# Kernel tuning notes

Measured on AMD Instinct MI355X. Metric: run time of the kernel, lower is better.

The kernel has to match this reference:

```python
import jax, jax.numpy as jnp
import numpy as np

NEG_SLOPE = 0.1  # leaky_relu slope used by Conv1dNormRelu in the repo


def grid_sample_bilinear(feat, xy):
    """Bilinear sample feat [B,C,H,W] at pixel coords xy [B,2,N].

    Equivalent to the repo's grid_sample_wrapper: it normalizes xy to [-1,1]
    and calls F.grid_sample(align_corners=True, padding_mode='zeros'), which
    maps back to exactly these pixel coordinates. Out-of-bounds corners -> 0.
    Returns [B,C,N].
    """
    B, C, H, W = feat.shape
    x = xy[:, 0]  # [B,N]
    y = xy[:, 1]
    x0 = jnp.floor(x)
    y0 = jnp.floor(y)
    wx1 = x - x0
    wy1 = y - y0
    wx0 = 1.0 - wx1
    wy0 = 1.0 - wy1

    def gather(ix, iy):
        valid = (ix >= 0) & (ix <= W - 1) & (iy >= 0) & (iy <= H - 1)
        ixc = jnp.clip(ix, 0, W - 1).astype(jnp.int32)
        iyc = jnp.clip(iy, 0, H - 1).astype(jnp.int32)
        # per-batch gather: f[:, iy, ix] -> [C, N]
        v = jax.vmap(lambda f, iy_, ix_: f[:, iy_, ix_])(feat, iyc, ixc)  # [B,C,N]
        return v * valid[:, None, :].astype(feat.dtype)

    out = (gather(x0, y0) * (wx0 * wy0)[:, None, :]
           + gather(x0 + 1, y0) * (wx1 * wy0)[:, None, :]
           + gather(x0, y0 + 1) * (wx0 * wy1)[:, None, :]
           + gather(x0 + 1, y0 + 1) * (wx1 * wy1)[:, None, :])
    return out


def setup_inputs() -> dict:
    key = jax.random.key(0)
    k1, k2, k3, k4 = jax.random.split(key, 4)
    B, N = 4, 16384
    C2D, C3D, H, W_img = 128, 128, 96, 160
    # pixel coords in [0, W-1] x [0, H-1]
    u = jax.random.uniform(k1, (B, 1, N), dtype=jnp.float32) * (W_img - 1)
    v = jax.random.uniform(k2, (B, 1, N), dtype=jnp.float32) * (H - 1)
    xy = jnp.concatenate([u, v], axis=1)  # [B,2,N]
    feat_2d = jax.random.normal(k3, (B, C2D, H, W_img), dtype=jnp.float32)
    feat_3d = jax.random.normal(k4, (B, C3D, N), dtype=jnp.float32)
    kw, kb = jax.random.split(jax.random.fold_in(key, 7))
    fan_in = C2D + C3D
    W = jax.random.normal(kw, (C3D, fan_in), dtype=jnp.float32) / np.sqrt(fan_in)
    b = jnp.zeros((C3D,), dtype=jnp.float32)
    return {"xy": xy, "feat_2d": feat_2d, "feat_3d": feat_3d, "W": W, "b": b}


def reference(xy, feat_2d, feat_3d, W, b):
    # torch.no_grad() around the gather -> stop_gradient
    feat_2d_to_3d = jax.lax.stop_gradient(grid_sample_bilinear(feat_2d, xy))  # [B,C2d,N]
    cat = jnp.concatenate([feat_2d_to_3d, feat_3d], axis=1)  # [B,C2d+C3d,N]
    # Conv1d with kernel_size=1 == pointwise matmul over channels
    y = jnp.einsum('oi,bin->bon', W, cat) + b[None, :, None]
    return jnp.where(y >= 0, y, NEG_SLOPE * y)
```

## Files before the change

kernel.cpp:

```cpp
#include <hip/hip_runtime.h>
#include <hip/hip_bf16.h>

#define NSAMP 16384
#define BB    4
#define C2D   128
#define C3D   128
#define HH    96
#define WW    160
#define COUT  128
#define KK    256
#define TN    64
#define HW    (HH*WW)
#define CATS  264

typedef __attribute__((ext_vector_type(8))) short bf16x8;
typedef __attribute__((ext_vector_type(4))) float f32x4;

__device__ __forceinline__ float bf16lo(unsigned int u) { return __uint_as_float(u << 16); }
__device__ __forceinline__ float bf16hi(unsigned int u) { return __uint_as_float(u & 0xffff0000u); }
__device__ __forceinline__ unsigned int pack2(float a, float b) {
    union { __hip_bfloat162 h; unsigned int u; } c;
    c.h = __float22bfloat162_rn(make_float2(a, b));
    return c.u;
}

__global__ __launch_bounds__(256) void transpose_cvt_kernel(
    const float* __restrict__ f2d, unsigned short* __restrict__ f2dt)
{
    __shared__ unsigned short t[64 * 66];
    const int tid  = threadIdx.x;
    const int lane = tid & 63;
    const int wv   = tid >> 6;
    const int blk  = blockIdx.x;
    const int b    = blk / ((HW / 64) * 2);
    const int rem  = blk % ((HW / 64) * 2);
    const int c0   = (rem & 1) * 64;
    const int hw0  = (rem >> 1) * 64;

    #pragma unroll
    for (int s = 0; s < 16; ++s) {
        const int cl = s * 4 + wv;
        float v = f2d[(size_t)(b * C2D + c0 + cl) * HW + hw0 + lane];
        __hip_bfloat16 h = __float2bfloat16(v);
        t[lane * 66 + cl] = *(unsigned short*)&h;
    }
    __syncthreads();
    const unsigned int* tw  = (const unsigned int*)t;
    unsigned int*       wsu = (unsigned int*)f2dt;
    #pragma unroll
    for (int s = 0; s < 8; ++s) {
        const int hwl = s * 8 + (tid >> 5);
        const int cu  = tid & 31;
        wsu[((size_t)(b * HW + hw0 + hwl) * C2D + c0) / 2 + cu] = tw[hwl * 33 + cu];
    }
}

__global__ __launch_bounds__(256) void wcvt_kernel(
    const float* __restrict__ Wm, unsigned short* __restrict__ Wb)
{
    const int i = blockIdx.x * 256 + threadIdx.x;
    const float4 v = ((const float4*)Wm)[i];
    uint2 o;
    o.x = pack2(v.x, v.y);
    o.y = pack2(v.z, v.w);
    ((uint2*)Wb)[i] = o;
}

__global__ __launch_bounds__(256, 4) void fuse_kernel(
    const float*          __restrict__ xy,
    const unsigned short* __restrict__ f2dt,
    const float*          __restrict__ f3d,
    const unsigned short* __restrict__ Wb,
    const float*          __restrict__ bias,
    float* __restrict__ out)
{
    __shared__ unsigned short cat[TN * CATS];
    __shared__ float4 sw4[TN];
    __shared__ int4   soff4[TN];

    const int tid  = threadIdx.x;
    const int lane = tid & 63;
    const int wv   = tid >> 6;
    const int blk  = blockIdx.x;
    const int b    = blk >> 8;
    const int n0   = (blk & 255) * TN;

    if (tid < TN) {
        const int n = n0 + tid;
        float x = xy[((size_t)b * 2 + 0) * NSAMP + n];
        float y = xy[((size_t)b * 2 + 1) * NSAMP + n];
        float xf = floorf(x), yf = floorf(y);
        float wx1 = x - xf, wy1 = y - yf;
        float wx0 = 1.0f - wx1, wy0 = 1.0f - wy1;
        int x0 = (int)xf, y0 = (int)yf;
        int x1 = x0 + 1, y1 = y0 + 1;
        if (x0 < 0 || x0 > WW - 1) wx0 = 0.0f;
        if (x1 < 0 || x1 > WW - 1) wx1 = 0.0f;
        if (y0 < 0 || y0 > HH - 1) wy0 = 0.0f;
        if (y1 < 0 || y1 > HH - 1) wy1 = 0.0f;
        x0 = min(max(x0, 0), WW - 1);
        x1 = min(max(x1, 0), WW - 1);
        y0 = min(max(y0, 0), HH - 1);
        y1 = min(max(y1, 0), HH - 1);
        sw4[tid]   = make_float4(wx0 * wy0, wx1 * wy0, wx0 * wy1, wx1 * wy1);
        soff4[tid] = make_int4(y0 * WW + x0, y0 * WW + x1,
                               y1 * WW + x0, y1 * WW + x1);
    }
    __syncthreads();

    unsigned int* catw = (unsigned int*)cat;

    {
        const float* p3 = f3d + (size_t)(b * C3D) * NSAMP + n0 + lane;
        #pragma unroll
        for (int ch = 0; ch < 4; ++ch) {
            const int cbase = wv * 32 + ch * 8;
            float v[8];
            #pragma unroll
            for (int t = 0; t < 8; ++t) v[t] = p3[(size_t)(cbase + t) * NSAMP];
            uint4 pk;
            pk.x = pack2(v[0], v[1]);
            pk.y = pack2(v[2], v[3]);
            pk.z = pack2(v[4], v[5]);
            pk.w = pack2(v[6], v[7]);
            *(uint4*)&catw[lane * (CATS / 2) + (C2D / 2) + (cbase >> 1)] = pk;
        }
    }

    {
        const int s   = lane >> 5;
        const int ch4 = (lane & 31) * 4;
        const unsigned short* fb = f2dt + (size_t)b * HW * C2D + ch4;
        #pragma unroll 4
        for (int i = 0; i < 8; ++i) {
            const int j = wv * 16 + i * 2 + s;
            const float4 w = sw4[j];
            const int4   o = soff4[j];
            const uint2 c0v = *(const uint2*)(fb + (size_t)o.x * C2D);
            const uint2 c1v = *(const uint2*)(fb + (size_t)o.y * C2D);
            const uint2 c2v = *(const uint2*)(fb + (size_t)o.z * C2D);
            const uint2 c3v = *(const uint2*)(fb + (size_t)o.w * C2D);
            float r0 = w.x * bf16lo(c0v.x) + w.y * bf16lo(c1v.x)
                     + w.z * bf16lo(c2v.x) + w.w * bf16lo(c3v.x);
            float r1 = w.x * bf16hi(c0v.x) + w.y * bf16hi(c1v.x)
                     + w.z * bf16hi(c2v.x) + w.w * bf16hi(c3v.x);
            float r2 = w.x * bf16lo(c0v.y) + w.y * bf16lo(c1v.y)
                     + w.z * bf16lo(c2v.y) + w.w * bf16lo(c3v.y);
            float r3 = w.x * bf16hi(c0v.y) + w.y * bf16hi(c1v.y)
                     + w.z * bf16hi(c2v.y) + w.w * bf16hi(c3v.y);
            uint2 pk;
            pk.x = pack2(r0, r1);
            pk.y = pack2(r2, r3);
            *(uint2*)&catw[j * (CATS / 2) + (ch4 >> 1)] = pk;
        }
    }
    __syncthreads();

    {
        const int quad = lane >> 4;
        const int nloc = lane & 15;

        f32x4 acc[2][4];
        #pragma unroll
        for (int mt = 0; mt < 2; ++mt)
            #pragma unroll
            for (int nt = 0; nt < 4; ++nt)
                acc[mt][nt] = (f32x4){0.f, 0.f, 0.f, 0.f};

        const unsigned short* wb0 = Wb + (size_t)(wv * 32 + nloc) * KK + quad * 8;

        #pragma unroll 2
        for (int ks = 0; ks < 8; ++ks) {
            const int k0 = ks * 32;
            const bf16x8 a0 = *(const bf16x8*)(wb0 + k0);
            const bf16x8 a1 = *(const bf16x8*)(wb0 + 16 * KK + k0);
            #pragma unroll
            for (int nt = 0; nt < 4; ++nt) {
                const bf16x8 bfrag = *(const bf16x8*)
                    &cat[(nt * 16 + nloc) * CATS + k0 + quad * 8];
                acc[0][nt] = __builtin_amdgcn_mfma_f32_16x16x32_bf16(
                    a0, bfrag, acc[0][nt], 0, 0, 0);
                acc[1][nt] = __builtin_amdgcn_mfma_f32_16x16x32_bf16(
                    a1, bfrag, acc[1][nt], 0, 0, 0);
            }
        }

        #pragma unroll
        for (int mt = 0; mt < 2; ++mt) {
            const int cobase = wv * 32 + mt * 16 + quad * 4;
            float bv[4];
            #pragma unroll
            for (int r = 0; r < 4; ++r) bv[r] = bias[cobase + r];
            #pragma unroll
            for (int nt = 0; nt < 4; ++nt) {
                float* po = out + (size_t)(b * COUT + cobase) * NSAMP
                          + n0 + nt * 16 + nloc;
                #pragma unroll
                for (int r = 0; r < 4; ++r) {
                    float yv = acc[mt][nt][r] + bv[r];
                    yv = (yv >= 0.0f) ? yv : 0.1f * yv;
                    po[(size_t)r * NSAMP] = yv;
                }
            }
        }
    }
}

extern "C" void kernel_launch(void* const* d_in, const int* in_sizes, int n_in,
                              void* d_out, int out_size, void* d_ws, size_t ws_size,
                              hipStream_t stream) {
    const float* xy   = (const float*)d_in[0];
    const float* f2d  = (const float*)d_in[1];
    const float* f3d  = (const float*)d_in[2];
    const float* Wm   = (const float*)d_in[3];
    const float* bias = (const float*)d_in[4];
    float* out = (float*)d_out;

    unsigned short* f2dt = (unsigned short*)d_ws;
    unsigned short* Wb   = f2dt + (size_t)BB * HW * C2D;

    wcvt_kernel<<<dim3((COUT * KK / 4) / 256), 256, 0, stream>>>(Wm, Wb);
    transpose_cvt_kernel<<<dim3(BB * (HW / 64) * 2), 256, 0, stream>>>(f2d, f2dt);
    fuse_kernel<<<dim3(BB * (NSAMP / TN)), 256, 0, stream>>>(
        xy, f2dt, f3d, Wb, bias, out);
}
```

Baseline: 128.6 us.

## Project 2D features before bilinear sampling and fuse interpolation into accumulators

Uses linearity of bilinear sampling to apply the 2D half of the pointwise weights to the image feature map first, producing a projected bf16 map. The fuse kernel then runs an MFMA only over the 3D features and adds bilinearly interpolated projected values directly into the accumulators, removing the shared-memory staging of sampled 2D features. The separate transpose kernel is replaced by the projection kernel, and the tile size drops to 32 samples with a block-order swizzle. Rounding the projected values to bf16 slightly changes the numerics.

Result: slower. 166.8 us (+29.7%).

```diff
diff --git a/kernel.cpp b/kernel.cpp
--- a/kernel.cpp
+++ b/kernel.cpp
@@ -8,10 +8,9 @@
 #define HH    96
 #define WW    160
 #define COUT  128
-#define KK    256
-#define TN    64
 #define HW    (HH*WW)
-#define CATS  264
+#define TN    32
+#define PROW  136
 
 typedef __attribute__((ext_vector_type(8))) short bf16x8;
 typedef __attribute__((ext_vector_type(4))) float f32x4;
@@ -24,66 +23,100 @@
     return c.u;
 }
 
-__global__ __launch_bounds__(256) void transpose_cvt_kernel(
-    const float* __restrict__ f2d, unsigned short* __restrict__ f2dt)
-{
-    __shared__ unsigned short t[64 * 66];
-    const int tid  = threadIdx.x;
-    const int lane = tid & 63;
-    const int wv   = tid >> 6;
-    const int blk  = blockIdx.x;
-    const int b    = blk / ((HW / 64) * 2);
-    const int rem  = blk % ((HW / 64) * 2);
-    const int c0   = (rem & 1) * 64;
-    const int hw0  = (rem >> 1) * 64;
-
-    #pragma unroll
-    for (int s = 0; s < 16; ++s) {
-        const int cl = s * 4 + wv;
-        float v = f2d[(size_t)(b * C2D + c0 + cl) * HW + hw0 + lane];
-        __hip_bfloat16 h = __float2bfloat16(v);
-        t[lane * 66 + cl] = *(unsigned short*)&h;
-    }
-    __syncthreads();
-    const unsigned int* tw  = (const unsigned int*)t;
-    unsigned int*       wsu = (unsigned int*)f2dt;
-    #pragma unroll
-    for (int s = 0; s < 8; ++s) {
-        const int hwl = s * 8 + (tid >> 5);
-        const int cu  = tid & 31;
-        wsu[((size_t)(b * HW + hw0 + hwl) * C2D + c0) / 2 + cu] = tw[hwl * 33 + cu];
-    }
-}
-
 __global__ __launch_bounds__(256) void wcvt_kernel(
-    const float* __restrict__ Wm, unsigned short* __restrict__ Wb)
+    const float* __restrict__ Wm,
+    unsigned short* __restrict__ Wb2, unsigned short* __restrict__ Wb3)
 {
     const int i = blockIdx.x * 256 + threadIdx.x;
     const float4 v = ((const float4*)Wm)[i];
     uint2 o;
     o.x = pack2(v.x, v.y);
     o.y = pack2(v.z, v.w);
-    ((uint2*)Wb)[i] = o;
-}
-
-__global__ __launch_bounds__(256, 4) void fuse_kernel(
-    const float*          __restrict__ xy,
-    const unsigned short* __restrict__ f2dt,
-    const float*          __restrict__ f3d,
-    const unsigned short* __restrict__ Wb,
-    const float*          __restrict__ bias,
-    float* __restrict__ out)
+    const int co = i >> 6;
+    const int c4 = i & 63;
+    unsigned short* dst = (c4 < 32) ? (Wb2 + co * 128 + c4 * 4)
+                                    : (Wb3 + co * 128 + (c4 - 32) * 4);
+    *(uint2*)dst = o;
+}
+
+__global__ __launch_bounds__(256, 4) void proj2d_kernel(
+    const float*          __restrict__ f2d,
+    const unsigned short* __restrict__ Wb2,
+    unsigned short*       __restrict__ P)
 {
-    __shared__ unsigned short cat[TN * CATS];
-    __shared__ float4 sw4[TN];
-    __shared__ int4   soff4[TN];
-
+    __shared__ unsigned short t[64 * PROW];
     const int tid  = threadIdx.x;
     const int lane = tid & 63;
     const int wv   = tid >> 6;
     const int blk  = blockIdx.x;
-    const int b    = blk >> 8;
-    const int n0   = (blk & 255) * TN;
+    const int b    = blk / (HW / 64);
+    const int hw0  = (blk % (HW / 64)) * 64;
+
+    const float* src = f2d + (size_t)b * C2D * HW + hw0 + lane;
+    #pragma unroll
+    for (int g = 0; g < 4; ++g) {
+        const int c0 = wv * 32 + g * 8;
+        float v[8];
+        #pragma unroll
+        for (int k = 0; k < 8; ++k) v[k] = src[(size_t)(c0 + k) * HW];
+        uint4 pk;
+        pk.x = pack2(v[0], v[1]);
+        pk.y = pack2(v[2], v[3]);
+        pk.z = pack2(v[4], v[5]);
+        pk.w = pack2(v[6], v[7]);
+        *(uint4*)&t[lane * PROW + c0] = pk;
+    }
+    __syncthreads();
+
+    const int quad = lane >> 4;
+    const int nloc = lane & 15;
+
+    f32x4 acc[8];
+    #pragma unroll
+    for (int nt = 0; nt < 8; ++nt) acc[nt] = (f32x4){0.f, 0.f, 0.f, 0.f};
+
+    const unsigned short* arow = &t[(wv * 16 + nloc) * PROW + quad * 8];
+    const unsigned short* brow = Wb2 + nloc * 128 + quad * 8;
+
+    #pragma unroll
+    for (int ks = 0; ks < 4; ++ks) {
+        const bf16x8 a = *(const bf16x8*)(arow + ks * 32);
+        #pragma unroll
+        for (int nt = 0; nt < 8; ++nt) {
+            const bf16x8 bb = *(const bf16x8*)(brow + nt * 16 * 128 + ks * 32);
+            acc[nt] = __builtin_amdgcn_mfma_f32_16x16x32_bf16(a, bb, acc[nt], 0, 0, 0);
+        }
+    }
+
+    unsigned short* pb = P + ((size_t)b * HW + hw0 + wv * 16 + quad * 4) * C2D + nloc;
+    #pragma unroll
+    for (int nt = 0; nt < 8; ++nt) {
+        #pragma unroll
+        for (int r = 0; r < 4; ++r) {
+            __hip_bfloat16 h = __float2bfloat16(acc[nt][r]);
+            pb[(size_t)r * C2D + nt * 16] = *(unsigned short*)&h;
+        }
+    }
+}
+
+__global__ __launch_bounds__(256, 6) void fuse_kernel(
+    const float*          __restrict__ xy,
+    const unsigned short* __restrict__ P,
+    const float*          __restrict__ f3d,
+    const unsigned short* __restrict__ Wb3,
+    const float*          __restrict__ bias,
+    float* __restrict__ out)
+{
+    __shared__ unsigned short cat3[TN * PROW];
+    __shared__ float4 sw4[TN];
+    __shared__ int4   soff4[TN];
+
+    const int tid  = threadIdx.x;
+    const int lane = tid & 63;
+    const int wv   = tid >> 6;
+    const int blk  = (blockIdx.x & 7) * 256 + (blockIdx.x >> 3);
+    const int b    = blk >> 9;
+    const int n0   = (blk & 511) * TN;
 
     if (tid < TN) {
         const int n = n0 + tid;
@@ -106,101 +139,95 @@
         soff4[tid] = make_int4(y0 * WW + x0, y0 * WW + x1,
                                y1 * WW + x0, y1 * WW + x1);
     }
+
+    {
+        const int s  = tid & 31;
+        const int cg = tid >> 5;
+        const float* p3 = f3d + ((size_t)(b * C3D + cg * 16)) * NSAMP + n0 + s;
+        float v[16];
+        #pragma unroll
+        for (int k = 0; k < 16; ++k) v[k] = p3[(size_t)k * NSAMP];
+        uint4 pk0, pk1;
+        pk0.x = pack2(v[0],  v[1]);  pk0.y = pack2(v[2],  v[3]);
+        pk0.z = pack2(v[4],  v[5]);  pk0.w = pack2(v[6],  v[7]);
+        pk1.x = pack2(v[8],  v[9]);  pk1.y = pack2(v[10], v[11]);
+        pk1.z = pack2(v[12], v[13]); pk1.w = pack2(v[14], v[15]);
+        *(uint4*)&cat3[s * PROW + cg * 16]     = pk0;
+        *(uint4*)&cat3[s * PROW + cg * 16 + 8] = pk1;
+    }
     __syncthreads();
 
-    unsigned int* catw = (unsigned int*)cat;
+    const int quad = lane >> 4;
+    const int nloc = lane & 15;
+
+    f32x4 acc[2][2];
+    #pragma unroll
+    for (int mt = 0; mt < 2; ++mt)
+        #pragma unroll
+        for (int nt = 0; nt < 2; ++nt)
+            acc[mt][nt] = (f32x4){0.f, 0.f, 0.f, 0.f};
 
     {
-        const float* p3 = f3d + (size_t)(b * C3D) * NSAMP + n0 + lane;
-        #pragma unroll
-        for (int ch = 0; ch < 4; ++ch) {
-            const int cbase = wv * 32 + ch * 8;
-            float v[8];
-            #pragma unroll
-            for (int t = 0; t < 8; ++t) v[t] = p3[(size_t)(cbase + t) * NSAMP];
-            uint4 pk;
-            pk.x = pack2(v[0], v[1]);
-            pk.y = pack2(v[2], v[3]);
-            pk.z = pack2(v[4], v[5]);
-            pk.w = pack2(v[6], v[7]);
-            *(uint4*)&catw[lane * (CATS / 2) + (C2D / 2) + (cbase >> 1)] = pk;
-        }
-    }
-
-    {
-        const int s   = lane >> 5;
-        const int ch4 = (lane & 31) * 4;
-        const unsigned short* fb = f2dt + (size_t)b * HW * C2D + ch4;
-        #pragma unroll 4
-        for (int i = 0; i < 8; ++i) {
-            const int j = wv * 16 + i * 2 + s;
-            const float4 w = sw4[j];
-            const int4   o = soff4[j];
-            const uint2 c0v = *(const uint2*)(fb + (size_t)o.x * C2D);
-            const uint2 c1v = *(const uint2*)(fb + (size_t)o.y * C2D);
-            const uint2 c2v = *(const uint2*)(fb + (size_t)o.z * C2D);
-            const uint2 c3v = *(const uint2*)(fb + (size_t)o.w * C2D);
-            float r0 = w.x * bf16lo(c0v.x) + w.y * bf16lo(c1v.x)
-                     + w.z * bf16lo(c2v.x) + w.w * bf16lo(c3v.x);
-            float r1 = w.x * bf16hi(c0v.x) + w.y * bf16hi(c1v.x)
-                     + w.z * bf16hi(c2v.x) + w.w * bf16hi(c3v.x);
-            float r2 = w.x * bf16lo(c0v.y) + w.y * bf16lo(c1v.y)
-                     + w.z * bf16lo(c2v.y) + w.w * bf16lo(c3v.y);
-            float r3 = w.x * bf16hi(c0v.y) + w.y * bf16hi(c1v.y)
-                     + w.z * bf16hi(c2v.y) + w.w * bf16hi(c3v.y);
-            uint2 pk;
-            pk.x = pack2(r0, r1);
-            pk.y = pack2(r2, r3);
-            *(uint2*)&catw[j * (CATS / 2) + (ch4 >> 1)] = pk;
-        }
-    }
-    __syncthreads();
-
-    {
-        const int quad = lane >> 4;
-        const int nloc = lane & 15;
-
-        f32x4 acc[2][4];
-        #pragma unroll
-        for (int mt = 0; mt < 2; ++mt)
-            #pragma unroll
-            for (int nt = 0; nt < 4; ++nt)
-                acc[mt][nt] = (f32x4){0.f, 0.f, 0.f, 0.f};
-
-        const unsigned short* wb0 = Wb + (size_t)(wv * 32 + nloc) * KK + quad * 8;
-
-        #pragma unroll 2
-        for (int ks = 0; ks < 8; ++ks) {
+        const unsigned short* wb0 = Wb3 + (wv * 32 + nloc) * 128 + quad * 8;
+        #pragma unroll
+        for (int ks = 0; ks < 4; ++ks) {
             const int k0 = ks * 32;
             const bf16x8 a0 = *(const bf16x8*)(wb0 + k0);
-            const bf16x8 a1 = *(const bf16x8*)(wb0 + 16 * KK + k0);
+            const bf16x8 a1 = *(const bf16x8*)(wb0 + 16 * 128 + k0);
             #pragma unroll
-            for (int nt = 0; nt < 4; ++nt) {
+            for (int nt = 0; nt < 2; ++nt) {
                 const bf16x8 bfrag = *(const bf16x8*)
-                    &cat[(nt * 16 + nloc) * CATS + k0 + quad * 8];
+                    &cat3[(nt * 16 + nloc) * PROW + k0 + quad * 8];
                 acc[0][nt] = __builtin_amdgcn_mfma_f32_16x16x32_bf16(
                     a0, bfrag, acc[0][nt], 0, 0, 0);
                 acc[1][nt] = __builtin_amdgcn_mfma_f32_16x16x32_bf16(
                     a1, bfrag, acc[1][nt], 0, 0, 0);
             }
         }
-
-        #pragma unroll
-        for (int mt = 0; mt < 2; ++mt) {
-            const int cobase = wv * 32 + mt * 16 + quad * 4;
-            float bv[4];
+    }
+
+    {
+        const unsigned short* pb = P + (size_t)b * HW * C2D;
+        #pragma unroll
+        for (int nt = 0; nt < 2; ++nt) {
+            const int j = nt * 16 + nloc;
+            const float4 w = sw4[j];
+            const int4   o = soff4[j];
             #pragma unroll
-            for (int r = 0; r < 4; ++r) bv[r] = bias[cobase + r];
+            for (int mt = 0; mt < 2; ++mt) {
+                const int cobase = wv * 32 + mt * 16 + quad * 4;
+                const unsigned short* pc = pb + cobase;
+                const uint2 c0v = *(const uint2*)(pc + (size_t)o.x * C2D);
+                const uint2 c1v = *(const uint2*)(pc + (size_t)o.y * C2D);
+                const uint2 c2v = *(const uint2*)(pc + (size_t)o.z * C2D);
+                const uint2 c3v = *(const uint2*)(pc + (size_t)o.w * C2D);
+                acc[mt][nt][0] += w.x * bf16lo(c0v.x) + w.y * bf16lo(c1v.x)
+                                + w.z * bf16lo(c2v.x) + w.w * bf16lo(c3v.x);
+                acc[mt][nt][1] += w.x * bf16hi(c0v.x) + w.y * bf16hi(c1v.x)
+                                + w.z * bf16hi(c2v.x) + w.w * bf16hi(c3v.x);
+                acc[mt][nt][2] += w.x * bf16lo(c0v.y) + w.y * bf16lo(c1v.y)
+                                + w.z * bf16lo(c2v.y) + w.w * bf16lo(c3v.y);
+                acc[mt][nt][3] += w.x * bf16hi(c0v.y) + w.y * bf16hi(c1v.y)
+                                + w.z * bf16hi(c2v.y) + w.w * bf16hi(c3v.y);
+            }
+        }
+    }
+
+    #pragma unroll
+    for (int mt = 0; mt < 2; ++mt) {
+        const int cobase = wv * 32 + mt * 16 + quad * 4;
+        float bv[4];
+        #pragma unroll
+        for (int r = 0; r < 4; ++r) bv[r] = bias[cobase + r];
+        #pragma unroll
+        for (int nt = 0; nt < 2; ++nt) {
+            float* po = out + (size_t)(b * COUT + cobase) * NSAMP
+                      + n0 + nt * 16 + nloc;
             #pragma unroll
-            for (int nt = 0; nt < 4; ++nt) {
-                float* po = out + (size_t)(b * COUT + cobase) * NSAMP
-                          + n0 + nt * 16 + nloc;
-                #pragma unroll
-                for (int r = 0; r < 4; ++r) {
-                    float yv = acc[mt][nt][r] + bv[r];
-                    yv = (yv >= 0.0f) ? yv : 0.1f * yv;
-                    po[(size_t)r * NSAMP] = yv;
-                }
+            for (int r = 0; r < 4; ++r) {
+                float yv = acc[mt][nt][r] + bv[r];
+                yv = (yv >= 0.0f) ? yv : 0.1f * yv;
+                po[(size_t)r * NSAMP] = yv;
             }
         }
     }
@@ -216,11 +243,12 @@
     const float* bias = (const float*)d_in[4];
     float* out = (float*)d_out;
 
-    unsigned short* f2dt = (unsigned short*)d_ws;
-    unsigned short* Wb   = f2dt + (size_t)BB * HW * C2D;
-
-    wcvt_kernel<<<dim3((COUT * KK / 4) / 256), 256, 0, stream>>>(Wm, Wb);
-    transpose_cvt_kernel<<<dim3(BB * (HW / 64) * 2), 256, 0, stream>>>(f2d, f2dt);
+    unsigned short* P   = (unsigned short*)d_ws;
+    unsigned short* Wb2 = P + (size_t)BB * HW * C2D;
+    unsigned short* Wb3 = Wb2 + (size_t)COUT * 128;
+
+    wcvt_kernel<<<dim3((COUT * 256 / 4) / 256), 256, 0, stream>>>(Wm, Wb2, Wb3);
+    proj2d_kernel<<<dim3(BB * (HW / 64)), 256, 0, stream>>>(f2d, Wb2, P);
     fuse_kernel<<<dim3(BB * (NSAMP / TN)), 256, 0, stream>>>(
-        xy, f2dt, f3d, Wb, bias, out);
-}
+        xy, P, f3d, Wb3, bias, out);
+}
```

## Overlap gather with MFMA on feat_3d half and widen kernels to 512 threads

Applied to the files above, without the earlier changes.

The fused kernel now runs 512 threads per block. Bilinear weights and offsets stay in registers and are broadcast with shuffles instead of going through shared memory. The MFMA over the feat_3d half of K runs while the 2D gather loads are in flight, and the 2D half is blended and multiplied after a second barrier. The transpose kernel is rewritten to handle 128 pixels by all channels per block with XOR-swizzled shared memory and 16-byte stores. Both kernels also remap block indices, presumably to spread consecutive blocks across XCDs. The cost is higher register pressure from the prefetched gathers and an extra barrier.

Result: slower. 135.5 us (+5.3%).

```diff
diff --git a/kernel.cpp b/kernel.cpp
--- a/kernel.cpp
+++ b/kernel.cpp
@@ -9,9 +9,10 @@
 #define WW    160
 #define COUT  128
 #define KK    256
+#define HW    (HH*WW)
 #define TN    64
-#define HW    (HH*WW)
 #define CATS  264
+#define TS    136
 
 typedef __attribute__((ext_vector_type(8))) short bf16x8;
 typedef __attribute__((ext_vector_type(4))) float f32x4;
@@ -24,37 +25,6 @@
     return c.u;
 }
 
-__global__ __launch_bounds__(256) void transpose_cvt_kernel(
-    const float* __restrict__ f2d, unsigned short* __restrict__ f2dt)
-{
-    __shared__ unsigned short t[64 * 66];
-    const int tid  = threadIdx.x;
-    const int lane = tid & 63;
-    const int wv   = tid >> 6;
-    const int blk  = blockIdx.x;
-    const int b    = blk / ((HW / 64) * 2);
-    const int rem  = blk % ((HW / 64) * 2);
-    const int c0   = (rem & 1) * 64;
-    const int hw0  = (rem >> 1) * 64;
-
-    #pragma unroll
-    for (int s = 0; s < 16; ++s) {
-        const int cl = s * 4 + wv;
-        float v = f2d[(size_t)(b * C2D + c0 + cl) * HW + hw0 + lane];
-        __hip_bfloat16 h = __float2bfloat16(v);
-        t[lane * 66 + cl] = *(unsigned short*)&h;
-    }
-    __syncthreads();
-    const unsigned int* tw  = (const unsigned int*)t;
-    unsigned int*       wsu = (unsigned int*)f2dt;
-    #pragma unroll
-    for (int s = 0; s < 8; ++s) {
-        const int hwl = s * 8 + (tid >> 5);
-        const int cu  = tid & 31;
-        wsu[((size_t)(b * HW + hw0 + hwl) * C2D + c0) / 2 + cu] = tw[hwl * 33 + cu];
-    }
-}
-
 __global__ __launch_bounds__(256) void wcvt_kernel(
     const float* __restrict__ Wm, unsigned short* __restrict__ Wb)
 {
@@ -66,7 +36,59 @@
     ((uint2*)Wb)[i] = o;
 }
 
-__global__ __launch_bounds__(256, 4) void fuse_kernel(
+__global__ __launch_bounds__(512) void transpose_cvt_kernel(
+    const float* __restrict__ f2d, unsigned short* __restrict__ f2dt)
+{
+    __shared__ unsigned short t[128 * TS];
+    unsigned int* tw = (unsigned int*)t;
+    const int tid  = threadIdx.x;
+    const int lane = tid & 63;
+    const int wv   = tid >> 6;
+    const int blk  = (blockIdx.x & 7) * 60 + (blockIdx.x >> 3);
+    const int b    = blk / 120;
+    const int hw0  = (blk % 120) * 128;
+
+    const int xk = 4 * ((lane >> 3) & 7);
+    const float* src = f2d + (size_t)b * C2D * HW + hw0 + lane;
+    #pragma unroll
+    for (int st = 0; st < 8; ++st) {
+        const int c = wv * 16 + st * 2;
+        const float va0 = src[(size_t)c * HW];
+        const float vb0 = src[(size_t)(c + 1) * HW];
+        const float va1 = src[(size_t)c * HW + 64];
+        const float vb1 = src[(size_t)(c + 1) * HW + 64];
+        const int w = (c >> 1) ^ xk;
+        tw[lane        * (TS / 2) + w] = pack2(va0, vb0);
+        tw[(lane + 64) * (TS / 2) + w] = pack2(va1, vb1);
+    }
+    __syncthreads();
+    #pragma unroll
+    for (int it = 0; it < 4; ++it) {
+        const int r  = it * 32 + (tid >> 4);
+        const int rk = 4 * ((r >> 3) & 7);
+        const uint4 v = *(const uint4*)&tw[r * (TS / 2) + (((tid & 15) * 4) ^ rk)];
+        *(uint4*)&f2dt[((size_t)b * HW + hw0 + r) * C2D + (tid & 15) * 8] = v;
+    }
+}
+
+__device__ __forceinline__ void blend_write(
+    const uint2* cv, const float4 bw, unsigned int* catw, int row, int ch4)
+{
+    float r0 = bw.x * bf16lo(cv[0].x) + bw.y * bf16lo(cv[1].x)
+             + bw.z * bf16lo(cv[2].x) + bw.w * bf16lo(cv[3].x);
+    float r1 = bw.x * bf16hi(cv[0].x) + bw.y * bf16hi(cv[1].x)
+             + bw.z * bf16hi(cv[2].x) + bw.w * bf16hi(cv[3].x);
+    float r2 = bw.x * bf16lo(cv[0].y) + bw.y * bf16lo(cv[1].y)
+             + bw.z * bf16lo(cv[2].y) + bw.w * bf16lo(cv[3].y);
+    float r3 = bw.x * bf16hi(cv[0].y) + bw.y * bf16hi(cv[1].y)
+             + bw.z * bf16hi(cv[2].y) + bw.w * bf16hi(cv[3].y);
+    uint2 pk;
+    pk.x = pack2(r0, r1);
+    pk.y = pack2(r2, r3);
+    *(uint2*)&catw[row * (CATS / 2) + (ch4 >> 1)] = pk;
+}
+
+__global__ __launch_bounds__(512, 4) void fuse_kernel(
     const float*          __restrict__ xy,
     const unsigned short* __restrict__ f2dt,
     const float*          __restrict__ f3d,
@@ -75,18 +97,19 @@
     float* __restrict__ out)
 {
     __shared__ unsigned short cat[TN * CATS];
-    __shared__ float4 sw4[TN];
-    __shared__ int4   soff4[TN];
+    unsigned int* catw = (unsigned int*)cat;
 
     const int tid  = threadIdx.x;
     const int lane = tid & 63;
     const int wv   = tid >> 6;
-    const int blk  = blockIdx.x;
+    const int blk  = (blockIdx.x & 7) * 128 + (blockIdx.x >> 3);
     const int b    = blk >> 8;
     const int n0   = (blk & 255) * TN;
 
-    if (tid < TN) {
-        const int n = n0 + tid;
+    float w4x, w4y, w4z, w4w;
+    int   o4x, o4y, o4z, o4w;
+    {
+        const int n = n0 + wv * 8 + (lane & 7);
         float x = xy[((size_t)b * 2 + 0) * NSAMP + n];
         float y = xy[((size_t)b * 2 + 1) * NSAMP + n];
         float xf = floorf(x), yf = floorf(y);
@@ -102,105 +125,127 @@
         x1 = min(max(x1, 0), WW - 1);
         y0 = min(max(y0, 0), HH - 1);
         y1 = min(max(y1, 0), HH - 1);
-        sw4[tid]   = make_float4(wx0 * wy0, wx1 * wy0, wx0 * wy1, wx1 * wy1);
-        soff4[tid] = make_int4(y0 * WW + x0, y0 * WW + x1,
-                               y1 * WW + x0, y1 * WW + x1);
+        w4x = wx0 * wy0; w4y = wx1 * wy0; w4z = wx0 * wy1; w4w = wx1 * wy1;
+        o4x = y0 * WW + x0; o4y = y0 * WW + x1;
+        o4z = y1 * WW + x0; o4w = y1 * WW + x1;
+    }
+
+    float v3[16];
+    {
+        const float* p3 = f3d + ((size_t)(b * C3D + wv * 16)) * NSAMP + n0 + lane;
+        #pragma unroll
+        for (int t = 0; t < 16; ++t) v3[t] = p3[(size_t)t * NSAMP];
+    }
+
+    const int s2  = lane >> 5;
+    const int ch4 = (lane & 31) * 4;
+    const unsigned short* fb = f2dt + (size_t)b * HW * C2D + ch4;
+    uint2  ga[2][4];
+    float4 wA[2];
+    #pragma unroll
+    for (int i = 0; i < 2; ++i) {
+        const int src = i * 2 + s2;
+        int4 o;
+        o.x = __shfl(o4x, src); o.y = __shfl(o4y, src);
+        o.z = __shfl(o4z, src); o.w = __shfl(o4w, src);
+        wA[i].x = __shfl(w4x, src); wA[i].y = __shfl(w4y, src);
+        wA[i].z = __shfl(w4z, src); wA[i].w = __shfl(w4w, src);
+        ga[i][0] = *(const uint2*)(fb + (size_t)o.x * C2D);
+        ga[i][1] = *(const uint2*)(fb + (size_t)o.y * C2D);
+        ga[i][2] = *(const uint2*)(fb + (size_t)o.z * C2D);
+        ga[i][3] = *(const uint2*)(fb + (size_t)o.w * C2D);
+    }
+
+    {
+        uint4 pk0, pk1;
+        pk0.x = pack2(v3[0],  v3[1]);  pk0.y = pack2(v3[2],  v3[3]);
+        pk0.z = pack2(v3[4],  v3[5]);  pk0.w = pack2(v3[6],  v3[7]);
+        pk1.x = pack2(v3[8],  v3[9]);  pk1.y = pack2(v3[10], v3[11]);
+        pk1.z = pack2(v3[12], v3[13]); pk1.w = pack2(v3[14], v3[15]);
+        *(uint4*)&catw[lane * (CATS / 2) + (C2D / 2) + wv * 8]     = pk0;
+        *(uint4*)&catw[lane * (CATS / 2) + (C2D / 2) + wv * 8 + 4] = pk1;
     }
     __syncthreads();
 
-    unsigned int* catw = (unsigned int*)cat;
-
-    {
-        const float* p3 = f3d + (size_t)(b * C3D) * NSAMP + n0 + lane;
-        #pragma unroll
-        for (int ch = 0; ch < 4; ++ch) {
-            const int cbase = wv * 32 + ch * 8;
-            float v[8];
+    const int quad = lane >> 4;
+    const int nloc = lane & 15;
+    const int mwv  = (wv & 3) * 32;
+    const int nwv  = (wv >> 2) * 32;
+
+    f32x4 acc[2][2];
+    #pragma unroll
+    for (int mt = 0; mt < 2; ++mt)
+        #pragma unroll
+        for (int nt = 0; nt < 2; ++nt)
+            acc[mt][nt] = (f32x4){0.f, 0.f, 0.f, 0.f};
+
+    const unsigned short* wb0 = Wb + (size_t)(mwv + nloc) * KK + quad * 8;
+
+    #pragma unroll
+    for (int ks = 4; ks < 8; ++ks) {
+        const int k0 = ks * 32;
+        const bf16x8 a0 = *(const bf16x8*)(wb0 + k0);
+        const bf16x8 a1 = *(const bf16x8*)(wb0 + 16 * KK + k0);
+        #pragma unroll
+        for (int nt = 0; nt < 2; ++nt) {
+            const bf16x8 bf = *(const bf16x8*)
+                &cat[(nwv + nt * 16 + nloc) * CATS + k0 + quad * 8];
+            acc[0][nt] = __builtin_amdgcn_mfma_f32_16x16x32_bf16(a0, bf, acc[0][nt], 0, 0, 0);
+            acc[1][nt] = __builtin_amdgcn_mfma_f32_16x16x32_bf16(a1, bf, acc[1][nt], 0, 0, 0);
+        }
+    }
+
+    uint2  gb[2][4];
+    float4 wB[2];
+    #pragma unroll
+    for (int i = 0; i < 2; ++i) {
+        const int src = (i + 2) * 2 + s2;
+        int4 o;
+        o.x = __shfl(o4x, src); o.y = __shfl(o4y, src);
+        o.z = __shfl(o4z, src); o.w = __shfl(o4w, src);
+        wB[i].x = __shfl(w4x, src); wB[i].y = __shfl(w4y, src);
+        wB[i].z = __shfl(w4z, src); wB[i].w = __shfl(w4w, src);
+        gb[i][0] = *(const uint2*)(fb + (size_t)o.x * C2D);
+        gb[i][1] = *(const uint2*)(fb + (size_t)o.y * C2D);
+        gb[i][2] = *(const uint2*)(fb + (size_t)o.z * C2D);
+        gb[i][3] = *(const uint2*)(fb + (size_t)o.w * C2D);
+        blend_write(ga[i], wA[i], catw, wv * 8 + i * 2 + s2, ch4);
+    }
+    #pragma unroll
+    for (int i = 0; i < 2; ++i) {
+        blend_write(gb[i], wB[i], catw, wv * 8 + (i + 2) * 2 + s2, ch4);
+    }
+    __syncthreads();
+
+    #pragma unroll
+    for (int ks = 0; ks < 4; ++ks) {
+        const int k0 = ks * 32;
+        const bf16x8 a0 = *(const bf16x8*)(wb0 + k0);
+        const bf16x8 a1 = *(const bf16x8*)(wb0 + 16 * KK + k0);
+        #pragma unroll
+        for (int nt = 0; nt < 2; ++nt) {
+            const bf16x8 bf = *(const bf16x8*)
+                &cat[(nwv + nt * 16 + nloc) * CATS + k0 + quad * 8];
+            acc[0][nt] = __builtin_amdgcn_mfma_f32_16x16x32_bf16(a0, bf, acc[0][nt], 0, 0, 0);
+            acc[1][nt] = __builtin_amdgcn_mfma_f32_16x16x32_bf16(a1, bf, acc[1][nt], 0, 0, 0);
+        }
+    }
+
+    #pragma unroll
+    for (int mt = 0; mt < 2; ++mt) {
+        const int cobase = mwv + mt * 16 + quad * 4;
+        float bv[4];
+        #pragma unroll
+        for (int r = 0; r < 4; ++r) bv[r] = bias[cobase + r];
+        #pragma unroll
+        for (int nt = 0; nt < 2; ++nt) {
+            float* po = out + (size_t)(b * COUT + cobase) * NSAMP
+                      + n0 + nwv + nt * 16 + nloc;
             #pragma unroll
-            for (int t = 0; t < 8; ++t) v[t] = p3[(size_t)(cbase + t) * NSAMP];
-            uint4 pk;
-            pk.x = pack2(v[0], v[1]);
-            pk.y = pack2(v[2], v[3]);
-            pk.z = pack2(v[4], v[5]);
-            pk.w = pack2(v[6], v[7]);
-            *(uint4*)&catw[lane * (CATS / 2) + (C2D / 2) + (cbase >> 1)] = pk;
-        }
-    }
-
-    {
-        const int s   = lane >> 5;
-        const int ch4 = (lane & 31) * 4;
-        const unsigned short* fb = f2dt + (size_t)b * HW * C2D + ch4;
-        #pragma unroll 4
-        for (int i = 0; i < 8; ++i) {
-            const int j = wv * 16 + i * 2 + s;
-            const float4 w = sw4[j];
-            const int4   o = soff4[j];
-            const uint2 c0v = *(const uint2*)(fb + (size_t)o.x * C2D);
-            const uint2 c1v = *(const uint2*)(fb + (size_t)o.y * C2D);
-            const uint2 c2v = *(const uint2*)(fb + (size_t)o.z * C2D);
-            const uint2 c3v = *(const uint2*)(fb + (size_t)o.w * C2D);
-            float r0 = w.x * bf16lo(c0v.x) + w.y * bf16lo(c1v.x)
-                     + w.z * bf16lo(c2v.x) + w.w * bf16lo(c3v.x);
-            float r1 = w.x * bf16hi(c0v.x) + w.y * bf16hi(c1v.x)
-                     + w.z * bf16hi(c2v.x) + w.w * bf16hi(c3v.x);
-            float r2 = w.x * bf16lo(c0v.y) + w.y * bf16lo(c1v.y)
-                     + w.z * bf16lo(c2v.y) + w.w * bf16lo(c3v.y);
-            float r3 = w.x * bf16hi(c0v.y) + w.y * bf16hi(c1v.y)
-                     + w.z * bf16hi(c2v.y) + w.w * bf16hi(c3v.y);
-            uint2 pk;
-            pk.x = pack2(r0, r1);
-            pk.y = pack2(r2, r3);
-            *(uint2*)&catw[j * (CATS / 2) + (ch4 >> 1)] = pk;
-        }
-    }
-    __syncthreads();
-
-    {
-        const int quad = lane >> 4;
-        const int nloc = lane & 15;
-
-        f32x4 acc[2][4];
-        #pragma unroll
-        for (int mt = 0; mt < 2; ++mt)
-            #pragma unroll
-            for (int nt = 0; nt < 4; ++nt)
-                acc[mt][nt] = (f32x4){0.f, 0.f, 0.f, 0.f};
-
-        const unsigned short* wb0 = Wb + (size_t)(wv * 32 + nloc) * KK + quad * 8;
-
-        #pragma unroll 2
-        for (int ks = 0; ks < 8; ++ks) {
-            const int k0 = ks * 32;
-            const bf16x8 a0 = *(const bf16x8*)(wb0 + k0);
-            const bf16x8 a1 = *(const bf16x8*)(wb0 + 16 * KK + k0);
-            #pragma unroll
-            for (int nt = 0; nt < 4; ++nt) {
-                const bf16x8 bfrag = *(const bf16x8*)
-                    &cat[(nt * 16 + nloc) * CATS + k0 + quad * 8];
-                acc[0][nt] = __builtin_amdgcn_mfma_f32_16x16x32_bf16(
-                    a0, bfrag, acc[0][nt], 0, 0, 0);
-                acc[1][nt] = __builtin_amdgcn_mfma_f32_16x16x32_bf16(
-                    a1, bfrag, acc[1][nt], 0, 0, 0);
-            }
-        }
-
-        #pragma unroll
-        for (int mt = 0; mt < 2; ++mt) {
-            const int cobase = wv * 32 + mt * 16 + quad * 4;
-            float bv[4];
-            #pragma unroll
-            for (int r = 0; r < 4; ++r) bv[r] = bias[cobase + r];
-            #pragma unroll
-            for (int nt = 0; nt < 4; ++nt) {
-                float* po = out + (size_t)(b * COUT + cobase) * NSAMP
-                          + n0 + nt * 16 + nloc;
-                #pragma unroll
-                for (int r = 0; r < 4; ++r) {
-                    float yv = acc[mt][nt][r] + bv[r];
-                    yv = (yv >= 0.0f) ? yv : 0.1f * yv;
-                    po[(size_t)r * NSAMP] = yv;
-                }
+            for (int r = 0; r < 4; ++r) {
+                float yv = acc[mt][nt][r] + bv[r];
+                yv = (yv >= 0.0f) ? yv : 0.1f * yv;
+                po[(size_t)r * NSAMP] = yv;
             }
         }
     }
@@ -220,7 +265,7 @@
     unsigned short* Wb   = f2dt + (size_t)BB * HW * C2D;
 
     wcvt_kernel<<<dim3((COUT * KK / 4) / 256), 256, 0, stream>>>(Wm, Wb);
-    transpose_cvt_kernel<<<dim3(BB * (HW / 64) * 2), 256, 0, stream>>>(f2d, f2dt);
-    fuse_kernel<<<dim3(BB * (NSAMP / TN)), 256, 0, stream>>>(
+    transpose_cvt_kernel<<<dim3(BB * (HW / 128)), 512, 0, stream>>>(f2d, f2dt);
+    fuse_kernel<<<dim3(BB * (NSAMP / TN)), 512, 0, stream>>>(
         xy, f2dt, f3d, Wb, bias, out);
 }
```

## Overlap bilinear gathers with feat_3d MFMA half and remap block order

Applied to the files above, without the earlier changes.

The fuse kernel now issues half of the bilinear gathers early, runs the MFMA steps over the feat_3d half of K while those loads are in flight, then blends and runs the feat_2d half. This aims to hide gather latency behind matrix work. The transpose kernel is rewritten to handle 128-pixel tiles of all channels with 512 threads, XOR-swizzled shared memory and 16-byte stores. Both kernels also remap block indices so that consecutive blocks land on different XCDs. More registers are held live across the MFMA phase, which may lower occupancy.

Result: no change. 128.8 us (+0.1%).

```diff
diff --git a/kernel.cpp b/kernel.cpp
--- a/kernel.cpp
+++ b/kernel.cpp
@@ -9,9 +9,10 @@
 #define WW    160
 #define COUT  128
 #define KK    256
+#define HW    (HH*WW)
 #define TN    64
-#define HW    (HH*WW)
 #define CATS  264
+#define TS    136
 
 typedef __attribute__((ext_vector_type(8))) short bf16x8;
 typedef __attribute__((ext_vector_type(4))) float f32x4;
@@ -24,37 +25,6 @@
     return c.u;
 }
 
-__global__ __launch_bounds__(256) void transpose_cvt_kernel(
-    const float* __restrict__ f2d, unsigned short* __restrict__ f2dt)
-{
-    __shared__ unsigned short t[64 * 66];
-    const int tid  = threadIdx.x;
-    const int lane = tid & 63;
-    const int wv   = tid >> 6;
-    const int blk  = blockIdx.x;
-    const int b    = blk / ((HW / 64) * 2);
-    const int rem  = blk % ((HW / 64) * 2);
-    const int c0   = (rem & 1) * 64;
-    const int hw0  = (rem >> 1) * 64;
-
-    #pragma unroll
-    for (int s = 0; s < 16; ++s) {
-        const int cl = s * 4 + wv;
-        float v = f2d[(size_t)(b * C2D + c0 + cl) * HW + hw0 + lane];
-        __hip_bfloat16 h = __float2bfloat16(v);
-        t[lane * 66 + cl] = *(unsigned short*)&h;
-    }
-    __syncthreads();
-    const unsigned int* tw  = (const unsigned int*)t;
-    unsigned int*       wsu = (unsigned int*)f2dt;
-    #pragma unroll
-    for (int s = 0; s < 8; ++s) {
-        const int hwl = s * 8 + (tid >> 5);
-        const int cu  = tid & 31;
-        wsu[((size_t)(b * HW + hw0 + hwl) * C2D + c0) / 2 + cu] = tw[hwl * 33 + cu];
-    }
-}
-
 __global__ __launch_bounds__(256) void wcvt_kernel(
     const float* __restrict__ Wm, unsigned short* __restrict__ Wb)
 {
@@ -64,6 +34,58 @@
     o.x = pack2(v.x, v.y);
     o.y = pack2(v.z, v.w);
     ((uint2*)Wb)[i] = o;
+}
+
+__global__ __launch_bounds__(512) void transpose_cvt_kernel(
+    const float* __restrict__ f2d, unsigned short* __restrict__ f2dt)
+{
+    __shared__ unsigned short t[128 * TS];
+    unsigned int* tw = (unsigned int*)t;
+    const int tid  = threadIdx.x;
+    const int lane = tid & 63;
+    const int wv   = tid >> 6;
+    const int blk  = (blockIdx.x & 7) * 60 + (blockIdx.x >> 3);
+    const int b    = blk / 120;
+    const int hw0  = (blk % 120) * 128;
+
+    const int xk = 4 * ((lane >> 3) & 7);
+    const float* src = f2d + (size_t)b * C2D * HW + hw0 + lane;
+    #pragma unroll
+    for (int st = 0; st < 8; ++st) {
+        const int c = wv * 16 + st * 2;
+        const float va0 = src[(size_t)c * HW];
+        const float vb0 = src[(size_t)(c + 1) * HW];
+        const float va1 = src[(size_t)c * HW + 64];
+        const float vb1 = src[(size_t)(c + 1) * HW + 64];
+        const int w = (c >> 1) ^ xk;
+        tw[lane        * (TS / 2) + w] = pack2(va0, vb0);
+        tw[(lane + 64) * (TS / 2) + w] = pack2(va1, vb1);
+    }
+    __syncthreads();
+    #pragma unroll
+    for (int it = 0; it < 4; ++it) {
+        const int r  = it * 32 + (tid >> 4);
+        const int rk = 4 * ((r >> 3) & 7);
+        const uint4 v = *(const uint4*)&tw[r * (TS / 2) + (((tid & 15) * 4) ^ rk)];
+        *(uint4*)&f2dt[((size_t)b * HW + hw0 + r) * C2D + (tid & 15) * 8] = v;
+    }
+}
+
+__device__ __forceinline__ void blend_write(
+    const uint2* cv, const float4 bw, unsigned int* catw, int row, int ch4)
+{
+    float r0 = bw.x * bf16lo(cv[0].x) + bw.y * bf16lo(cv[1].x)
+             + bw.z * bf16lo(cv[2].x) + bw.w * bf16lo(cv[3].x);
+    float r1 = bw.x * bf16hi(cv[0].x) + bw.y * bf16hi(cv[1].x)
+             + bw.z * bf16hi(cv[2].x) + bw.w * bf16hi(cv[3].x);
+    float r2 = bw.x * bf16lo(cv[0].y) + bw.y * bf16lo(cv[1].y)
+             + bw.z * bf16lo(cv[2].y) + bw.w * bf16lo(cv[3].y);
+    float r3 = bw.x * bf16hi(cv[0].y) + bw.y * bf16hi(cv[1].y)
+             + bw.z * bf16hi(cv[2].y) + bw.w * bf16hi(cv[3].y);
+    uint2 pk;
+    pk.x = pack2(r0, r1);
+    pk.y = pack2(r2, r3);
+    *(uint2*)&catw[row * (CATS / 2) + (ch4 >> 1)] = pk;
 }
 
 __global__ __launch_bounds__(256, 4) void fuse_kernel(
@@ -77,11 +99,12 @@
     __shared__ unsigned short cat[TN * CATS];
     __shared__ float4 sw4[TN];
     __shared__ int4   soff4[TN];
+    unsigned int* catw = (unsigned int*)cat;
 
     const int tid  = threadIdx.x;
     const int lane = tid & 63;
     const int wv   = tid >> 6;
-    const int blk  = blockIdx.x;
+    const int blk  = (blockIdx.x & 7) * 128 + (blockIdx.x >> 3);
     const int b    = blk >> 8;
     const int n0   = (blk & 255) * TN;
 
@@ -106,9 +129,6 @@
         soff4[tid] = make_int4(y0 * WW + x0, y0 * WW + x1,
                                y1 * WW + x0, y1 * WW + x1);
     }
-    __syncthreads();
-
-    unsigned int* catw = (unsigned int*)cat;
 
     {
         const float* p3 = f3d + (size_t)(b * C3D) * NSAMP + n0 + lane;
@@ -126,81 +146,98 @@
             *(uint4*)&catw[lane * (CATS / 2) + (C2D / 2) + (cbase >> 1)] = pk;
         }
     }
-
-    {
-        const int s   = lane >> 5;
-        const int ch4 = (lane & 31) * 4;
-        const unsigned short* fb = f2dt + (size_t)b * HW * C2D + ch4;
-        #pragma unroll 4
-        for (int i = 0; i < 8; ++i) {
-            const int j = wv * 16 + i * 2 + s;
-            const float4 w = sw4[j];
-            const int4   o = soff4[j];
-            const uint2 c0v = *(const uint2*)(fb + (size_t)o.x * C2D);
-            const uint2 c1v = *(const uint2*)(fb + (size_t)o.y * C2D);
-            const uint2 c2v = *(const uint2*)(fb + (size_t)o.z * C2D);
-            const uint2 c3v = *(const uint2*)(fb + (size_t)o.w * C2D);
-            float r0 = w.x * bf16lo(c0v.x) + w.y * bf16lo(c1v.x)
-                     + w.z * bf16lo(c2v.x) + w.w * bf16lo(c3v.x);
-            float r1 = w.x * bf16hi(c0v.x) + w.y * bf16hi(c1v.x)
-                     + w.z * bf16hi(c2v.x) + w.w * bf16hi(c3v.x);
-            float r2 = w.x * bf16lo(c0v.y) + w.y * bf16lo(c1v.y)
-                     + w.z * bf16lo(c2v.y) + w.w * bf16lo(c3v.y);
-            float r3 = w.x * bf16hi(c0v.y) + w.y * bf16hi(c1v.y)
-                     + w.z * bf16hi(c2v.y) + w.w * bf16hi(c3v.y);
-            uint2 pk;
-            pk.x = pack2(r0, r1);
-            pk.y = pack2(r2, r3);
-            *(uint2*)&catw[j * (CATS / 2) + (ch4 >> 1)] = pk;
-        }
-    }
     __syncthreads();
 
-    {
-        const int quad = lane >> 4;
-        const int nloc = lane & 15;
-
-        f32x4 acc[2][4];
-        #pragma unroll
-        for (int mt = 0; mt < 2; ++mt)
+    const int quad = lane >> 4;
+    const int nloc = lane & 15;
+    const int s2   = lane >> 5;
+    const int ch4  = (lane & 31) * 4;
+    const unsigned short* fb = f2dt + (size_t)b * HW * C2D + ch4;
+
+    uint2  ga[4][4];
+    float4 wA[4];
+    #pragma unroll
+    for (int i = 0; i < 4; ++i) {
+        const int j = wv * 16 + i * 2 + s2;
+        const int4 o = soff4[j];
+        wA[i] = sw4[j];
+        ga[i][0] = *(const uint2*)(fb + (size_t)o.x * C2D);
+        ga[i][1] = *(const uint2*)(fb + (size_t)o.y * C2D);
+        ga[i][2] = *(const uint2*)(fb + (size_t)o.z * C2D);
+        ga[i][3] = *(const uint2*)(fb + (size_t)o.w * C2D);
+    }
+
+    f32x4 acc[2][4];
+    #pragma unroll
+    for (int mt = 0; mt < 2; ++mt)
+        #pragma unroll
+        for (int nt = 0; nt < 4; ++nt)
+            acc[mt][nt] = (f32x4){0.f, 0.f, 0.f, 0.f};
+
+    const unsigned short* wb0 = Wb + (size_t)(wv * 32 + nloc) * KK + quad * 8;
+
+    #pragma unroll
+    for (int ks = 4; ks < 8; ++ks) {
+        const int k0 = ks * 32;
+        const bf16x8 a0 = *(const bf16x8*)(wb0 + k0);
+        const bf16x8 a1 = *(const bf16x8*)(wb0 + 16 * KK + k0);
+        #pragma unroll
+        for (int nt = 0; nt < 4; ++nt) {
+            const bf16x8 bfrag = *(const bf16x8*)
+                &cat[(nt * 16 + nloc) * CATS + k0 + quad * 8];
+            acc[0][nt] = __builtin_amdgcn_mfma_f32_16x16x32_bf16(
+                a0, bfrag, acc[0][nt], 0, 0, 0);
+            acc[1][nt] = __builtin_amdgcn_mfma_f32_16x16x32_bf16(
+                a1, bfrag, acc[1][nt], 0, 0, 0);
+        }
+    }
+
+    #pragma unroll
+    for (int i = 0; i < 4; ++i) {
+        const int j2 = wv * 16 + 8 + i * 2 + s2;
+        const int4 o = soff4[j2];
+        const float4 wv4 = sw4[j2];
+        uint2 gb[4];
+        gb[0] = *(const uint2*)(fb + (size_t)o.x * C2D);
+        gb[1] = *(const uint2*)(fb + (size_t)o.y * C2D);
+        gb[2] = *(const uint2*)(fb + (size_t)o.z * C2D);
+        gb[3] = *(const uint2*)(fb + (size_t)o.w * C2D);
+        blend_write(ga[i], wA[i], catw, wv * 16 + i * 2 + s2, ch4);
+        blend_write(gb, wv4, catw, j2, ch4);
+    }
+    __syncthreads();
+
+    #pragma unroll
+    for (int ks = 0; ks < 4; ++ks) {
+        const int k0 = ks * 32;
+        const bf16x8 a0 = *(const bf16x8*)(wb0 + k0);
+        const bf16x8 a1 = *(const bf16x8*)(wb0 + 16 * KK + k0);
+        #pragma unroll
+        for (int nt = 0; nt < 4; ++nt) {
+            const bf16x8 bfrag = *(const bf16x8*)
+                &cat[(nt * 16 + nloc) * CATS + k0 + quad * 8];
+            acc[0][nt] = __builtin_amdgcn_mfma_f32_16x16x32_bf16(
+                a0, bfrag, acc[0][nt], 0, 0, 0);
+            acc[1][nt] = __builtin_amdgcn_mfma_f32_16x16x32_bf16(
+                a1, bfrag, acc[1][nt], 0, 0, 0);
+        }
+    }
+
+    #pragma unroll
+    for (int mt = 0; mt < 2; ++mt) {
+        const int cobase = wv * 32 + mt * 16 + quad * 4;
+        float bv[4];
+        #pragma unroll
+        for (int r = 0; r < 4; ++r) bv[r] = bias[cobase + r];
+        #pragma unroll
+        for (int nt = 0; nt < 4; ++nt) {
+            float* po = out + (size_t)(b * COUT + cobase) * NSAMP
+                      + n0 + nt * 16 + nloc;
             #pragma unroll
-            for (int nt = 0; nt < 4; ++nt)
-                acc[mt][nt] = (f32x4){0.f, 0.f, 0.f, 0.f};
-
-        const unsigned short* wb0 = Wb + (size_t)(wv * 32 + nloc) * KK + quad * 8;
-
-        #pragma unroll 2
-        for (int ks = 0; ks < 8; ++ks) {
-            const int k0 = ks * 32;
-            const bf16x8 a0 = *(const bf16x8*)(wb0 + k0);
-            const bf16x8 a1 = *(const bf16x8*)(wb0 + 16 * KK + k0);
-            #pragma unroll
-            for (int nt = 0; nt < 4; ++nt) {
-                const bf16x8 bfrag = *(const bf16x8*)
-                    &cat[(nt * 16 + nloc) * CATS + k0 + quad * 8];
-                acc[0][nt] = __builtin_amdgcn_mfma_f32_16x16x32_bf16(
-                    a0, bfrag, acc[0][nt], 0, 0, 0);
-                acc[1][nt] = __builtin_amdgcn_mfma_f32_16x16x32_bf16(
-                    a1, bfrag, acc[1][nt], 0, 0, 0);
-            }
-        }
-
-        #pragma unroll
-        for (int mt = 0; mt < 2; ++mt) {
-            const int cobase = wv * 32 + mt * 16 + quad * 4;
-            float bv[4];
-            #pragma unroll
-            for (int r = 0; r < 4; ++r) bv[r] = bias[cobase + r];
-            #pragma unroll
-            for (int nt = 0; nt < 4; ++nt) {
-                float* po = out + (size_t)(b * COUT + cobase) * NSAMP
-                          + n0 + nt * 16 + nloc;
-                #pragma unroll
-                for (int r = 0; r < 4; ++r) {
-                    float yv = acc[mt][nt][r] + bv[r];
-                    yv = (yv >= 0.0f) ? yv : 0.1f * yv;
-                    po[(size_t)r * NSAMP] = yv;
-                }
+            for (int r = 0; r < 4; ++r) {
+                float yv = acc[mt][nt][r] + bv[r];
+                yv = (yv >= 0.0f) ? yv : 0.1f * yv;
+                po[(size_t)r * NSAMP] = yv;
             }
         }
     }
@@ -220,7 +257,7 @@
     unsigned short* Wb   = f2dt + (size_t)BB * HW * C2D;
 
     wcvt_kernel<<<dim3((COUT * KK / 4) / 256), 256, 0, stream>>>(Wm, Wb);
-    transpose_cvt_kernel<<<dim3(BB * (HW / 64) * 2), 256, 0, stream>>>(f2d, f2dt);
+    transpose_cvt_kernel<<<dim3(BB * (HW / 128)), 512, 0, stream>>>(f2d, f2dt);
     fuse_kernel<<<dim3(BB * (NSAMP / TN)), 256, 0, stream>>>(
         xy, f2dt, f3d, Wb, bias, out);
 }
```
